# Kernel optimization log

Measured on AMD Instinct MI355X. Metric: run time of the kernel, lower is better.

Reference implementation:

```python
import jax, jax.numpy as jnp
import numpy as np

N_AA = 20
A = 15
D_FEAT = 128
CA_IDX = 1
NUM_FUNCS = 3
FREQ_BANDS = jnp.array([1.0, 2.0, 3.0, 1.0, 0.5, 1.0 / 3.0], dtype=jnp.float32)


def setup_inputs() -> dict:
    key = jax.random.key(0)
    ks = jax.random.split(key, 16)
    b, L = 16, 1024
    d_in = D_FEAT + N_AA * A * 3 + 3 * (NUM_FUNCS * 2 * 2 + 1) + D_FEAT  # 1195
    inp = {
        "seq": jax.random.randint(ks[0], (b, L), 0, N_AA),
        "xyz": jax.random.normal(ks[1], (b, L, A, 3), dtype=jnp.float32),
        "dihedrals": jax.random.normal(ks[2], (b, L, 3), dtype=jnp.float32),
        "chain_idx": jax.random.randint(ks[3], (b, L), 0, 10),
        "orientation": jax.random.normal(ks[4], (b, L, 3, 3), dtype=jnp.float32),
        "atom_mask": jnp.ones((b, L, A), dtype=bool),
        "aa_emb": jax.random.normal(ks[5], (N_AA, D_FEAT), dtype=jnp.float32),
        "chain_emb": jax.random.normal(ks[6], (10, D_FEAT), dtype=jnp.float32).at[0].set(0.0),  # padding_idx=0
        "W1": jax.random.normal(ks[7], (d_in, 2 * D_FEAT), dtype=jnp.float32) * 0.02,
        "b1": jnp.zeros((2 * D_FEAT,), dtype=jnp.float32),
        "W2": jax.random.normal(ks[8], (2 * D_FEAT, D_FEAT), dtype=jnp.float32) * 0.02,
        "b2": jnp.zeros((D_FEAT,), dtype=jnp.float32),
        "W3": jax.random.normal(ks[9], (D_FEAT, D_FEAT), dtype=jnp.float32) * 0.02,
        "b3": jnp.zeros((D_FEAT,), dtype=jnp.float32),
        "W4": jax.random.normal(ks[10], (D_FEAT, D_FEAT), dtype=jnp.float32) * 0.02,
        "b4": jnp.zeros((D_FEAT,), dtype=jnp.float32),
    }
    return inp


def angular_encoding(x):
    # x: (..., d_in) -> (..., d_in * 13)
    xe = x[..., None]  # (..., d_in, 1)
    enc = jnp.concatenate([xe, jnp.sin(FREQ_BANDS * xe), jnp.cos(FREQ_BANDS * xe)], axis=-1)
    return enc.reshape(*x.shape[:-1], -1)


def reference(seq, xyz, dihedrals, chain_idx, orientation, atom_mask,
              aa_emb, chain_emb, W1, b1, W2, b2, W3, b3, W4, b4):
    b, L = seq.shape
    aa_type_feat = aa_emb[seq]  # (b, L, d_feat)

    # local coordinates relative to CA, rotated into local frame via O^T
    xyz_rel = xyz - xyz[:, :, CA_IDX:CA_IDX + 1, :]  # (b, L, A, 3)
    xyz_local = jnp.einsum('blji,blaj->blai', orientation, xyz_rel)  # O^T @ xyz_rel

    # one-hot select: place xyz_local in the slot of the residue's aa type
    onehot = jax.nn.one_hot(seq, N_AA, dtype=xyz.dtype)  # (b, L, 20)
    coord_feat = (onehot[:, :, :, None, None] * xyz_local[:, :, None, :, :]).reshape(b, L, N_AA * A * 3)

    dihedral_feat = angular_encoding(dihedrals)  # (b, L, 39)

    chain_feat = chain_emb[chain_idx] * (chain_idx != 0)[..., None].astype(xyz.dtype)  # padding_idx=0

    x = jnp.concatenate([aa_type_feat, coord_feat, dihedral_feat, chain_feat], axis=-1)
    h = jax.nn.relu(x @ W1 + b1)
    h = jax.nn.relu(h @ W2 + b2)
    h = jax.nn.relu(h @ W3 + b3)
    return h @ W4 + b4
```

## Files before the change

kernel.cpp:

```cpp
#include <hip/hip_runtime.h>
#include <math.h>

#define N_AA    20
#define NATOM   15
#define TM      16
#define MAXBL   16384
#define MAXBLK  (MAXBL / TM + N_AA)
#define NWAVE   16

#define FSX  104
#define HSX  264
#define H2SX 136

typedef __attribute__((ext_vector_type(8))) short bf16x8;
typedef __attribute__((ext_vector_type(4))) float f32x4;

#define W1F_SLOTS  (N_AA * 16 * 3 * 64)
#define W2F_SLOTS  (8 * 8 * 64)
#define W34F_SLOTS (8 * 4 * 64)
#define TOT_SLOTS  (W1F_SLOTS + W2F_SLOTS + 2 * W34F_SLOTS)

__device__ __forceinline__ unsigned short f2bf(float x) {
    unsigned u = __float_as_uint(x);
    return (unsigned short)((u + 0x7FFFu + ((u >> 16) & 1u)) >> 16);
}
__device__ __forceinline__ float bf2f(unsigned short h) {
    return __uint_as_float(((unsigned)h) << 16);
}
__device__ __forceinline__ void put2(unsigned short* H, unsigned short* L, int idx, float v) {
    unsigned short hi = f2bf(v);
    H[idx] = hi;
    L[idx] = f2bf(v - bf2f(hi));
}

__global__ __launch_bounds__(1024) void prep_kernel(
    const int* __restrict__ seq, const float* __restrict__ aa_emb,
    const float* __restrict__ chain_emb, const float* __restrict__ W1,
    const float* __restrict__ W2, const float* __restrict__ W3, const float* __restrict__ W4,
    int BL,
    float* __restrict__ aaT, float* __restrict__ chT,
    int* __restrict__ bucket_start, int* __restrict__ blk_type,
    int* __restrict__ blk_chunk, int* __restrict__ rowidx,
    unsigned short* __restrict__ W1fH, unsigned short* __restrict__ W1fL,
    unsigned short* __restrict__ W2fH, unsigned short* __restrict__ W2fL,
    unsigned short* __restrict__ W3fH, unsigned short* __restrict__ W3fL,
    unsigned short* __restrict__ W4fH, unsigned short* __restrict__ W4fL)
{
    const int t = threadIdx.x;
    const int b = blockIdx.x;

    if (b < 8) {
        const int tab = b * 4 + (t >> 8);
        const int col = t & 255;
        if (tab < 30) {
            if (tab < N_AA) {
                const float* e = aa_emb + tab * 128;
                float acc = 0.f;
                #pragma unroll 8
                for (int k = 0; k < 128; ++k)
                    acc += e[k] * W1[(size_t)k * 256 + col];
                aaT[tab * 256 + col] = acc;
            } else {
                const int c = tab - N_AA;
                const float* e = chain_emb + c * 128;
                float acc = 0.f;
                #pragma unroll 8
                for (int k = 0; k < 128; ++k)
                    acc += e[k] * W1[(size_t)(1067 + k) * 256 + col];
                chT[c * 256 + col] = acc;
            }
        }
        return;
    }

    if (b >= 9) {
        const int slot = (b - 9) * 1024 + t;
        if (slot >= TOT_SLOTS) return;
        float v[8];
        unsigned short *dH, *dL;
        if (slot < W1F_SLOTS) {
            const int g = slot / 3072, r1 = slot % 3072;
            const int tile = r1 / 192, chunk = (r1 / 64) % 3, lane = r1 % 64;
            const int n  = tile * 16 + (lane & 15);
            const int kb = chunk * 32 + (lane >> 4) * 8;
            #pragma unroll
            for (int j = 0; j < 8; ++j) {
                const int k = kb + j;
                float x = 0.f;
                if (k < 45)       x = W1[(size_t)(128 + g * 45 + k) * 256 + n];
                else if (k < 84)  x = W1[(size_t)(1028 + k - 45) * 256 + n];
                v[j] = x;
            }
            dH = W1fH + (size_t)slot * 8; dL = W1fL + (size_t)slot * 8;
        } else if (slot < W1F_SLOTS + W2F_SLOTS) {
            const int s = slot - W1F_SLOTS;
            const int tile = s / 512, chunk = (s / 64) % 8, lane = s % 64;
            const int n  = tile * 16 + (lane & 15);
            const int kb = chunk * 32 + (lane >> 4) * 8;
            #pragma unroll
            for (int j = 0; j < 8; ++j) v[j] = W2[(size_t)(kb + j) * 128 + n];
            dH = W2fH + (size_t)s * 8; dL = W2fL + (size_t)s * 8;
        } else if (slot < W1F_SLOTS + W2F_SLOTS + W34F_SLOTS) {
            const int s = slot - W1F_SLOTS - W2F_SLOTS;
            const int tile = s / 256, chunk = (s / 64) % 4, lane = s % 64;
            const int n  = tile * 16 + (lane & 15);
            const int kb = chunk * 32 + (lane >> 4) * 8;
            #pragma unroll
            for (int j = 0; j < 8; ++j) v[j] = W3[(size_t)(kb + j) * 128 + n];
            dH = W3fH + (size_t)s * 8; dL = W3fL + (size_t)s * 8;
        } else {
            const int s = slot - W1F_SLOTS - W2F_SLOTS - W34F_SLOTS;
            const int tile = s / 256, chunk = (s / 64) % 4, lane = s % 64;
            const int n  = tile * 16 + (lane & 15);
            const int kb = chunk * 32 + (lane >> 4) * 8;
            #pragma unroll
            for (int j = 0; j < 8; ++j) v[j] = W4[(size_t)(kb + j) * 128 + n];
            dH = W4fH + (size_t)s * 8; dL = W4fL + (size_t)s * 8;
        }
        #pragma unroll
        for (int j = 0; j < 8; ++j) {
            const unsigned short hi = f2bf(v[j]);
            dH[j] = hi;
            dL[j] = f2bf(v[j] - bf2f(hi));
        }
        return;
    }

    __shared__ int sseq[MAXBL];
    __shared__ int hist[NWAVE][N_AA];
    __shared__ int wcur[NWAVE][N_AA];
    __shared__ int bs[N_AA + 1];
    __shared__ int blkoff[N_AA + 1];

    const int w = t >> 6;
    for (int i = t; i < BL; i += 1024) sseq[i] = seq[i];
    if (t < NWAVE * N_AA) hist[t / N_AA][t % N_AA] = 0;
    __syncthreads();
    for (int i = t; i < BL; i += 1024) atomicAdd(&hist[w][sseq[i]], 1);
    __syncthreads();
    if (t == 0) {
        int runr = 0, runb = 0;
        for (int g = 0; g < N_AA; ++g) {
            int s = 0;
            #pragma unroll
            for (int ww = 0; ww < NWAVE; ++ww) s += hist[ww][g];
            bs[g] = runr; runr += s;
            blkoff[g] = runb; runb += (s + TM - 1) / TM;
        }
        bs[N_AA] = runr; blkoff[N_AA] = runb;
    }
    __syncthreads();
    if (t <= N_AA) bucket_start[t] = bs[t];
    if (t < NWAVE * N_AA) {
        const int w2 = t / N_AA, g2 = t % N_AA;
        int o = bs[g2];
        for (int ww = 0; ww < w2; ++ww) o += hist[ww][g2];
        wcur[w2][g2] = o;
    }
    const int nblk = blkoff[N_AA];
    for (int i = t; i < MAXBLK; i += 1024) {
        if (i < nblk) {
            int g = 0;
            while (blkoff[g + 1] <= i) ++g;
            blk_type[i]  = g;
            blk_chunk[i] = i - blkoff[g];
        } else blk_type[i] = -1;
    }
    __syncthreads();
    for (int i = t; i < BL; i += 1024) {
        const int pos = atomicAdd(&wcur[w][sseq[i]], 1);
        rowidx[pos] = i;
    }
}

__global__ __launch_bounds__(256, 5) void fused_kernel(
    const int* __restrict__ chain_idx, const float* __restrict__ xyz,
    const float* __restrict__ dihedrals, const float* __restrict__ orientation,
    const float* __restrict__ b1, const float* __restrict__ b2,
    const float* __restrict__ b3, const float* __restrict__ b4,
    const float* __restrict__ aaT, const float* __restrict__ chT,
    const int* __restrict__ bucket_start, const int* __restrict__ blk_type,
    const int* __restrict__ blk_chunk, const int* __restrict__ rowidx,
    const unsigned short* __restrict__ W1fH, const unsigned short* __restrict__ W1fL,
    const unsigned short* __restrict__ W2fH, const unsigned short* __restrict__ W2fL,
    const unsigned short* __restrict__ W3fH, const unsigned short* __restrict__ W3fL,
    const unsigned short* __restrict__ W4fH, const unsigned short* __restrict__ W4fL,
    float* __restrict__ out)
{
    __shared__ __align__(16) unsigned short smemA[2 * TM * HSX];
    __shared__ __align__(16) unsigned short smemB[2 * TM * H2SX];
    __shared__ int s_row[TM], s_rowld[TM], s_chain[TM];

    unsigned short* hAH   = smemA;
    unsigned short* hAL   = smemA + TM * HSX;
    unsigned short* featH = smemB;
    unsigned short* featL = smemB + TM * FSX;
    unsigned short* hBH   = smemB;
    unsigned short* hBL   = smemB + TM * H2SX;

    const int t = threadIdx.x;
    const int g = blk_type[blockIdx.x];
    if (g < 0) return;
    const int chunk  = blk_chunk[blockIdx.x];
    const int bstart = bucket_start[g] + chunk * TM;
    const int nrows  = min(TM, bucket_start[g + 1] - bstart);

    if (t < TM) {
        const bool valid = (t < nrows);
        const int rl = rowidx[valid ? (bstart + t) : bstart];
        s_row[t]   = valid ? rl : -1;
        s_rowld[t] = rl;
        s_chain[t] = chain_idx[rl];
    }
    __syncthreads();

    if (t < TM * NATOM) {
        const int r = t / NATOM, a = t % NATOM;
        const int rl = s_rowld[r];
        const float* xr = xyz + (size_t)rl * (NATOM * 3);
        const float cax = xr[3], cay = xr[4], caz = xr[5];
        const float rx = xr[a*3+0] - cax;
        const float ry = xr[a*3+1] - cay;
        const float rz = xr[a*3+2] - caz;
        const float* O = orientation + (size_t)rl * 9;
        put2(featH, featL, r * FSX + a*3 + 0, O[0]*rx + O[3]*ry + O[6]*rz);
        put2(featH, featL, r * FSX + a*3 + 1, O[1]*rx + O[4]*ry + O[7]*rz);
        put2(featH, featL, r * FSX + a*3 + 2, O[2]*rx + O[5]*ry + O[8]*rz);
    }
    if (t < TM * 3) {
        const int r = t / 3, d = t % 3;
        const float x = dihedrals[(size_t)s_rowld[r] * 3 + d];
        const int base = r * FSX + 45 + d * 13;
        const float F3 = (float)(1.0 / 3.0);
        const float s1 = sinf(x), c1 = cosf(x);
        put2(featH, featL, base + 0, x);
        put2(featH, featL, base + 1, s1);           put2(featH, featL, base + 2, sinf(2.f*x));
        put2(featH, featL, base + 3, sinf(3.f*x));  put2(featH, featL, base + 4, s1);
        put2(featH, featL, base + 5, sinf(0.5f*x)); put2(featH, featL, base + 6, sinf(F3*x));
        put2(featH, featL, base + 7, c1);           put2(featH, featL, base + 8, cosf(2.f*x));
        put2(featH, featL, base + 9, cosf(3.f*x));  put2(featH, featL, base +10, c1);
        put2(featH, featL, base +11, cosf(0.5f*x)); put2(featH, featL, base +12, cosf(F3*x));
    }
    if (t < TM) {
        #pragma unroll
        for (int k = 84; k < 96; ++k) { featH[t * FSX + k] = 0; featL[t * FSX + k] = 0; }
    }
    __syncthreads();

    const int wave = t >> 6, lane = t & 63, quad = lane >> 4, nid = lane & 15;
    const f32x4 zero = {0.f, 0.f, 0.f, 0.f};

    {
        f32x4 acc[4] = {zero, zero, zero, zero};
        for (int c = 0; c < 3; ++c) {
            const bf16x8 aH = *(const bf16x8*)(featH + nid * FSX + c * 32 + quad * 8);
            const bf16x8 aL = *(const bf16x8*)(featL + nid * FSX + c * 32 + quad * 8);
            #pragma unroll
            for (int tt = 0; tt < 4; ++tt) {
                const size_t off = ((size_t)((g * 16 + (wave * 4 + tt)) * 3 + c) * 64 + lane) * 8;
                const bf16x8 bH = *(const bf16x8*)(W1fH + off);
                const bf16x8 bL = *(const bf16x8*)(W1fL + off);
                acc[tt] = __builtin_amdgcn_mfma_f32_16x16x32_bf16(aH, bH, acc[tt], 0, 0, 0);
                acc[tt] = __builtin_amdgcn_mfma_f32_16x16x32_bf16(aH, bL, acc[tt], 0, 0, 0);
                acc[tt] = __builtin_amdgcn_mfma_f32_16x16x32_bf16(aL, bH, acc[tt], 0, 0, 0);
            }
        }
        #pragma unroll
        for (int tt = 0; tt < 4; ++tt) {
            const int j = (wave * 4 + tt) * 16 + nid;
            const float cb = b1[j] + aaT[g * 256 + j];
            #pragma unroll
            for (int r = 0; r < 4; ++r) {
                const int row = quad * 4 + r;
                float v = acc[tt][r] + cb + chT[s_chain[row] * 256 + j];
                v = fmaxf(v, 0.f);
                put2(hAH, hAL, row * HSX + j, v);
            }
        }
    }
    __syncthreads();

    {
        f32x4 acc[2] = {zero, zero};
        for (int c = 0; c < 8; ++c) {
            const bf16x8 aH = *(const bf16x8*)(hAH + nid * HSX + c * 32 + quad * 8);
            const bf16x8 aL = *(const bf16x8*)(hAL + nid * HSX + c * 32 + quad * 8);
            #pragma unroll
            for (int tt = 0; tt < 2; ++tt) {
                const size_t off = ((size_t)((wave * 2 + tt) * 8 + c) * 64 + lane) * 8;
                const bf16x8 bH = *(const bf16x8*)(W2fH + off);
                const bf16x8 bL = *(const bf16x8*)(W2fL + off);
                acc[tt] = __builtin_amdgcn_mfma_f32_16x16x32_bf16(aH, bH, acc[tt], 0, 0, 0);
                acc[tt] = __builtin_amdgcn_mfma_f32_16x16x32_bf16(aH, bL, acc[tt], 0, 0, 0);
                acc[tt] = __builtin_amdgcn_mfma_f32_16x16x32_bf16(aL, bH, acc[tt], 0, 0, 0);
            }
        }
        __syncthreads();
        #pragma unroll
        for (int tt = 0; tt < 2; ++tt) {
            const int j = (wave * 2 + tt) * 16 + nid;
            const float bb = b2[j];
            #pragma unroll
            for (int r = 0; r < 4; ++r) {
                const int row = quad * 4 + r;
                float v = fmaxf(acc[tt][r] + bb, 0.f);
                put2(hBH, hBL, row * H2SX + j, v);
            }
        }
    }
    __syncthreads();

    {
        f32x4 acc[2] = {zero, zero};
        for (int c = 0; c < 4; ++c) {
            const bf16x8 aH = *(const bf16x8*)(hBH + nid * H2SX + c * 32 + quad * 8);
            const bf16x8 aL = *(const bf16x8*)(hBL + nid * H2SX + c * 32 + quad * 8);
            #pragma unroll
            for (int tt = 0; tt < 2; ++tt) {
                const size_t off = ((size_t)((wave * 2 + tt) * 4 + c) * 64 + lane) * 8;
                const bf16x8 bH = *(const bf16x8*)(W3fH + off);
                const bf16x8 bL = *(const bf16x8*)(W3fL + off);
                acc[tt] = __builtin_amdgcn_mfma_f32_16x16x32_bf16(aH, bH, acc[tt], 0, 0, 0);
                acc[tt] = __builtin_amdgcn_mfma_f32_16x16x32_bf16(aH, bL, acc[tt], 0, 0, 0);
                acc[tt] = __builtin_amdgcn_mfma_f32_16x16x32_bf16(aL, bH, acc[tt], 0, 0, 0);
            }
        }
        #pragma unroll
        for (int tt = 0; tt < 2; ++tt) {
            const int j = (wave * 2 + tt) * 16 + nid;
            const float bb = b3[j];
            #pragma unroll
            for (int r = 0; r < 4; ++r) {
                const int row = quad * 4 + r;
                float v = fmaxf(acc[tt][r] + bb, 0.f);
                put2(hAH, hAL, row * HSX + j, v);
            }
        }
    }
    __syncthreads();

    {
        f32x4 acc[2] = {zero, zero};
        for (int c = 0; c < 4; ++c) {
            const bf16x8 aH = *(const bf16x8*)(hAH + nid * HSX + c * 32 + quad * 8);
            const bf16x8 aL = *(const bf16x8*)(hAL + nid * HSX + c * 32 + quad * 8);
            #pragma unroll
            for (int tt = 0; tt < 2; ++tt) {
                const size_t off = ((size_t)((wave * 2 + tt) * 4 + c) * 64 + lane) * 8;
                const bf16x8 bH = *(const bf16x8*)(W4fH + off);
                const bf16x8 bL = *(const bf16x8*)(W4fL + off);
                acc[tt] = __builtin_amdgcn_mfma_f32_16x16x32_bf16(aH, bH, acc[tt], 0, 0, 0);
                acc[tt] = __builtin_amdgcn_mfma_f32_16x16x32_bf16(aH, bL, acc[tt], 0, 0, 0);
                acc[tt] = __builtin_amdgcn_mfma_f32_16x16x32_bf16(aL, bH, acc[tt], 0, 0, 0);
            }
        }
        #pragma unroll
        for (int tt = 0; tt < 2; ++tt) {
            const int j = (wave * 2 + tt) * 16 + nid;
            const float bb = b4[j];
            #pragma unroll
            for (int r = 0; r < 4; ++r) {
                const int row = quad * 4 + r;
                const int orow = s_row[row];
                if (orow >= 0) out[(size_t)orow * 128 + j] = acc[tt][r] + bb;
            }
        }
    }
}

extern "C" void kernel_launch(void* const* d_in, const int* in_sizes, int n_in,
                              void* d_out, int out_size, void* d_ws, size_t ws_size,
                              hipStream_t stream) {
    const int*   seq    = (const int*)d_in[0];
    const float* xyz    = (const float*)d_in[1];
    const float* dihed  = (const float*)d_in[2];
    const int*   chain  = (const int*)d_in[3];
    const float* orient = (const float*)d_in[4];
    const float* aa_emb = (const float*)d_in[6];
    const float* ch_emb = (const float*)d_in[7];
    const float* W1 = (const float*)d_in[8];
    const float* b1 = (const float*)d_in[9];
    const float* W2 = (const float*)d_in[10];
    const float* b2 = (const float*)d_in[11];
    const float* W3 = (const float*)d_in[12];
    const float* b3 = (const float*)d_in[13];
    const float* W4 = (const float*)d_in[14];
    const float* b4 = (const float*)d_in[15];
    float* out = (float*)d_out;

    const int BL = in_sizes[0];

    char* p = (char*)d_ws;
    float* aaT = (float*)p;            p += 20 * 256 * 4;
    float* chT = (float*)p;            p += 10 * 256 * 4;
    int* bucket_start = (int*)p;       p += 32 * 4;
    int* blk_type     = (int*)p;       p += MAXBLK * 4;
    int* blk_chunk    = (int*)p;       p += MAXBLK * 4;
    int* rowidx       = (int*)p;       p += MAXBL * 4;
    p += ((16 - ((uintptr_t)p & 15)) & 15);
    unsigned short* W1fH = (unsigned short*)p; p += (size_t)W1F_SLOTS * 8 * 2;
    unsigned short* W1fL = (unsigned short*)p; p += (size_t)W1F_SLOTS * 8 * 2;
    unsigned short* W2fH = (unsigned short*)p; p += (size_t)W2F_SLOTS * 8 * 2;
    unsigned short* W2fL = (unsigned short*)p; p += (size_t)W2F_SLOTS * 8 * 2;
    unsigned short* W3fH = (unsigned short*)p; p += (size_t)W34F_SLOTS * 8 * 2;
    unsigned short* W3fL = (unsigned short*)p; p += (size_t)W34F_SLOTS * 8 * 2;
    unsigned short* W4fH = (unsigned short*)p; p += (size_t)W34F_SLOTS * 8 * 2;
    unsigned short* W4fL = (unsigned short*)p;

    const int nprep  = 9 + (TOT_SLOTS + 1023) / 1024;
    const int nfused = BL / TM + N_AA;

    prep_kernel<<<nprep, 1024, 0, stream>>>(seq, aa_emb, ch_emb, W1, W2, W3, W4, BL,
                                            aaT, chT, bucket_start, blk_type, blk_chunk, rowidx,
                                            W1fH, W1fL, W2fH, W2fL, W3fH, W3fL, W4fH, W4fL);
    fused_kernel<<<nfused, 256, 0, stream>>>(chain, xyz, dihed, orient,
                                             b1, b2, b3, b4, aaT, chT,
                                             bucket_start, blk_type, blk_chunk, rowidx,
                                             W1fH, W1fL, W2fH, W2fL, W3fH, W3fL, W4fH, W4fL,
                                             out);
}
```

Before: 124.4 us.

## Double row tile to 32 and reuse weight fragments across two row tiles

Raises the per-block row tile from 16 to 32 and the block size from 256 to 512 threads (8 waves). Each wave now loads each weight fragment once and applies it to two 16-row A tiles, with the column tiles redistributed across waves in every layer. The aim is to halve global/L2 weight traffic per output row and cut the number of blocks. The cost is more padded rows per amino-acid bucket, doubled shared memory per block, and higher register pressure from the doubled accumulators.

After: 124.2 us. No clear change (-0.2%).

```diff
diff --git a/kernel.cpp b/kernel.cpp
--- a/kernel.cpp
+++ b/kernel.cpp
@@ -3,7 +3,7 @@
 
 #define N_AA    20
 #define NATOM   15
-#define TM      16
+#define TM      32
 #define MAXBL   16384
 #define MAXBLK  (MAXBL / TM + N_AA)
 #define NWAVE   16
@@ -173,7 +173,7 @@
     }
 }
 
-__global__ __launch_bounds__(256, 5) void fused_kernel(
+__global__ __launch_bounds__(512, 4) void fused_kernel(
     const int* __restrict__ chain_idx, const float* __restrict__ xyz,
     const float* __restrict__ dihedrals, const float* __restrict__ orientation,
     const float* __restrict__ b1, const float* __restrict__ b2,
@@ -251,30 +251,38 @@
     const f32x4 zero = {0.f, 0.f, 0.f, 0.f};
 
     {
-        f32x4 acc[4] = {zero, zero, zero, zero};
+        f32x4 acc[2][2] = {{zero, zero}, {zero, zero}};
         for (int c = 0; c < 3; ++c) {
-            const bf16x8 aH = *(const bf16x8*)(featH + nid * FSX + c * 32 + quad * 8);
-            const bf16x8 aL = *(const bf16x8*)(featL + nid * FSX + c * 32 + quad * 8);
-            #pragma unroll
-            for (int tt = 0; tt < 4; ++tt) {
-                const size_t off = ((size_t)((g * 16 + (wave * 4 + tt)) * 3 + c) * 64 + lane) * 8;
+            const bf16x8 aH0 = *(const bf16x8*)(featH + nid * FSX + c * 32 + quad * 8);
+            const bf16x8 aL0 = *(const bf16x8*)(featL + nid * FSX + c * 32 + quad * 8);
+            const bf16x8 aH1 = *(const bf16x8*)(featH + (16 + nid) * FSX + c * 32 + quad * 8);
+            const bf16x8 aL1 = *(const bf16x8*)(featL + (16 + nid) * FSX + c * 32 + quad * 8);
+            #pragma unroll
+            for (int tt = 0; tt < 2; ++tt) {
+                const size_t off = ((size_t)((g * 16 + (wave * 2 + tt)) * 3 + c) * 64 + lane) * 8;
                 const bf16x8 bH = *(const bf16x8*)(W1fH + off);
                 const bf16x8 bL = *(const bf16x8*)(W1fL + off);
-                acc[tt] = __builtin_amdgcn_mfma_f32_16x16x32_bf16(aH, bH, acc[tt], 0, 0, 0);
-                acc[tt] = __builtin_amdgcn_mfma_f32_16x16x32_bf16(aH, bL, acc[tt], 0, 0, 0);
-                acc[tt] = __builtin_amdgcn_mfma_f32_16x16x32_bf16(aL, bH, acc[tt], 0, 0, 0);
-            }
-        }
-        #pragma unroll
-        for (int tt = 0; tt < 4; ++tt) {
-            const int j = (wave * 4 + tt) * 16 + nid;
+                acc[0][tt] = __builtin_amdgcn_mfma_f32_16x16x32_bf16(aH0, bH, acc[0][tt], 0, 0, 0);
+                acc[0][tt] = __builtin_amdgcn_mfma_f32_16x16x32_bf16(aH0, bL, acc[0][tt], 0, 0, 0);
+                acc[0][tt] = __builtin_amdgcn_mfma_f32_16x16x32_bf16(aL0, bH, acc[0][tt], 0, 0, 0);
+                acc[1][tt] = __builtin_amdgcn_mfma_f32_16x16x32_bf16(aH1, bH, acc[1][tt], 0, 0, 0);
+                acc[1][tt] = __builtin_amdgcn_mfma_f32_16x16x32_bf16(aH1, bL, acc[1][tt], 0, 0, 0);
+                acc[1][tt] = __builtin_amdgcn_mfma_f32_16x16x32_bf16(aL1, bH, acc[1][tt], 0, 0, 0);
+            }
+        }
+        #pragma unroll
+        for (int tt = 0; tt < 2; ++tt) {
+            const int j = (wave * 2 + tt) * 16 + nid;
             const float cb = b1[j] + aaT[g * 256 + j];
             #pragma unroll
-            for (int r = 0; r < 4; ++r) {
-                const int row = quad * 4 + r;
-                float v = acc[tt][r] + cb + chT[s_chain[row] * 256 + j];
-                v = fmaxf(v, 0.f);
-                put2(hAH, hAL, row * HSX + j, v);
+            for (int rt = 0; rt < 2; ++rt) {
+                #pragma unroll
+                for (int r = 0; r < 4; ++r) {
+                    const int row = rt * 16 + quad * 4 + r;
+                    float v = acc[rt][tt][r] + cb + chT[s_chain[row] * 256 + j];
+                    v = fmaxf(v, 0.f);
+                    put2(hAH, hAL, row * HSX + j, v);
+                }
             }
         }
     }
@@ -283,27 +291,29 @@
     {
         f32x4 acc[2] = {zero, zero};
         for (int c = 0; c < 8; ++c) {
-            const bf16x8 aH = *(const bf16x8*)(hAH + nid * HSX + c * 32 + quad * 8);
-            const bf16x8 aL = *(const bf16x8*)(hAL + nid * HSX + c * 32 + quad * 8);
-            #pragma unroll
-            for (int tt = 0; tt < 2; ++tt) {
-                const size_t off = ((size_t)((wave * 2 + tt) * 8 + c) * 64 + lane) * 8;
-                const bf16x8 bH = *(const bf16x8*)(W2fH + off);
-                const bf16x8 bL = *(const bf16x8*)(W2fL + off);
-                acc[tt] = __builtin_amdgcn_mfma_f32_16x16x32_bf16(aH, bH, acc[tt], 0, 0, 0);
-                acc[tt] = __builtin_amdgcn_mfma_f32_16x16x32_bf16(aH, bL, acc[tt], 0, 0, 0);
-                acc[tt] = __builtin_amdgcn_mfma_f32_16x16x32_bf16(aL, bH, acc[tt], 0, 0, 0);
-            }
+            const bf16x8 aH0 = *(const bf16x8*)(hAH + nid * HSX + c * 32 + quad * 8);
+            const bf16x8 aL0 = *(const bf16x8*)(hAL + nid * HSX + c * 32 + quad * 8);
+            const bf16x8 aH1 = *(const bf16x8*)(hAH + (16 + nid) * HSX + c * 32 + quad * 8);
+            const bf16x8 aL1 = *(const bf16x8*)(hAL + (16 + nid) * HSX + c * 32 + quad * 8);
+            const size_t off = ((size_t)(wave * 8 + c) * 64 + lane) * 8;
+            const bf16x8 bH = *(const bf16x8*)(W2fH + off);
+            const bf16x8 bL = *(const bf16x8*)(W2fL + off);
+            acc[0] = __builtin_amdgcn_mfma_f32_16x16x32_bf16(aH0, bH, acc[0], 0, 0, 0);
+            acc[0] = __builtin_amdgcn_mfma_f32_16x16x32_bf16(aH0, bL, acc[0], 0, 0, 0);
+            acc[0] = __builtin_amdgcn_mfma_f32_16x16x32_bf16(aL0, bH, acc[0], 0, 0, 0);
+            acc[1] = __builtin_amdgcn_mfma_f32_16x16x32_bf16(aH1, bH, acc[1], 0, 0, 0);
+            acc[1] = __builtin_amdgcn_mfma_f32_16x16x32_bf16(aH1, bL, acc[1], 0, 0, 0);
+            acc[1] = __builtin_amdgcn_mfma_f32_16x16x32_bf16(aL1, bH, acc[1], 0, 0, 0);
         }
         __syncthreads();
-        #pragma unroll
-        for (int tt = 0; tt < 2; ++tt) {
-            const int j = (wave * 2 + tt) * 16 + nid;
-            const float bb = b2[j];
+        const int j = wave * 16 + nid;
+        const float bb = b2[j];
+        #pragma unroll
+        for (int rt = 0; rt < 2; ++rt) {
             #pragma unroll
             for (int r = 0; r < 4; ++r) {
-                const int row = quad * 4 + r;
-                float v = fmaxf(acc[tt][r] + bb, 0.f);
+                const int row = rt * 16 + quad * 4 + r;
+                float v = fmaxf(acc[rt][r] + bb, 0.f);
                 put2(hBH, hBL, row * H2SX + j, v);
             }
         }
@@ -313,26 +323,28 @@
     {
         f32x4 acc[2] = {zero, zero};
         for (int c = 0; c < 4; ++c) {
-            const bf16x8 aH = *(const bf16x8*)(hBH + nid * H2SX + c * 32 + quad * 8);
-            const bf16x8 aL = *(const bf16x8*)(hBL + nid * H2SX + c * 32 + quad * 8);
-            #pragma unroll
-            for (int tt = 0; tt < 2; ++tt) {
-                const size_t off = ((size_t)((wave * 2 + tt) * 4 + c) * 64 + lane) * 8;
-                const bf16x8 bH = *(const bf16x8*)(W3fH + off);
-                const bf16x8 bL = *(const bf16x8*)(W3fL + off);
-                acc[tt] = __builtin_amdgcn_mfma_f32_16x16x32_bf16(aH, bH, acc[tt], 0, 0, 0);
-                acc[tt] = __builtin_amdgcn_mfma_f32_16x16x32_bf16(aH, bL, acc[tt], 0, 0, 0);
-                acc[tt] = __builtin_amdgcn_mfma_f32_16x16x32_bf16(aL, bH, acc[tt], 0, 0, 0);
-            }
-        }
-        #pragma unroll
-        for (int tt = 0; tt < 2; ++tt) {
-            const int j = (wave * 2 + tt) * 16 + nid;
-            const float bb = b3[j];
+            const bf16x8 aH0 = *(const bf16x8*)(hBH + nid * H2SX + c * 32 + quad * 8);
+            const bf16x8 aL0 = *(const bf16x8*)(hBL + nid * H2SX + c * 32 + quad * 8);
+            const bf16x8 aH1 = *(const bf16x8*)(hBH + (16 + nid) * H2SX + c * 32 + quad * 8);
+            const bf16x8 aL1 = *(const bf16x8*)(hBL + (16 + nid) * H2SX + c * 32 + quad * 8);
+            const size_t off = ((size_t)(wave * 4 + c) * 64 + lane) * 8;
+            const bf16x8 bH = *(const bf16x8*)(W3fH + off);
+            const bf16x8 bL = *(const bf16x8*)(W3fL + off);
+            acc[0] = __builtin_amdgcn_mfma_f32_16x16x32_bf16(aH0, bH, acc[0], 0, 0, 0);
+            acc[0] = __builtin_amdgcn_mfma_f32_16x16x32_bf16(aH0, bL, acc[0], 0, 0, 0);
+            acc[0] = __builtin_amdgcn_mfma_f32_16x16x32_bf16(aL0, bH, acc[0], 0, 0, 0);
+            acc[1] = __builtin_amdgcn_mfma_f32_16x16x32_bf16(aH1, bH, acc[1], 0, 0, 0);
+            acc[1] = __builtin_amdgcn_mfma_f32_16x16x32_bf16(aH1, bL, acc[1], 0, 0, 0);
+            acc[1] = __builtin_amdgcn_mfma_f32_16x16x32_bf16(aL1, bH, acc[1], 0, 0, 0);
+        }
+        const int j = wave * 16 + nid;
+        const float bb = b3[j];
+        #pragma unroll
+        for (int rt = 0; rt < 2; ++rt) {
             #pragma unroll
             for (int r = 0; r < 4; ++r) {
-                const int row = quad * 4 + r;
-                float v = fmaxf(acc[tt][r] + bb, 0.f);
+                const int row = rt * 16 + quad * 4 + r;
+                float v = fmaxf(acc[rt][r] + bb, 0.f);
                 put2(hAH, hAL, row * HSX + j, v);
             }
         }
@@ -342,27 +354,29 @@
     {
         f32x4 acc[2] = {zero, zero};
         for (int c = 0; c < 4; ++c) {
-            const bf16x8 aH = *(const bf16x8*)(hAH + nid * HSX + c * 32 + quad * 8);
-            const bf16x8 aL = *(const bf16x8*)(hAL + nid * HSX + c * 32 + quad * 8);
-            #pragma unroll
-            for (int tt = 0; tt < 2; ++tt) {
-                const size_t off = ((size_t)((wave * 2 + tt) * 4 + c) * 64 + lane) * 8;
-                const bf16x8 bH = *(const bf16x8*)(W4fH + off);
-                const bf16x8 bL = *(const bf16x8*)(W4fL + off);
-                acc[tt] = __builtin_amdgcn_mfma_f32_16x16x32_bf16(aH, bH, acc[tt], 0, 0, 0);
-                acc[tt] = __builtin_amdgcn_mfma_f32_16x16x32_bf16(aH, bL, acc[tt], 0, 0, 0);
-                acc[tt] = __builtin_amdgcn_mfma_f32_16x16x32_bf16(aL, bH, acc[tt], 0, 0, 0);
-            }
-        }
-        #pragma unroll
-        for (int tt = 0; tt < 2; ++tt) {
-            const int j = (wave * 2 + tt) * 16 + nid;
-            const float bb = b4[j];
+            const bf16x8 aH0 = *(const bf16x8*)(hAH + nid * HSX + c * 32 + quad * 8);
+            const bf16x8 aL0 = *(const bf16x8*)(hAL + nid * HSX + c * 32 + quad * 8);
+            const bf16x8 aH1 = *(const bf16x8*)(hAH + (16 + nid) * HSX + c * 32 + quad * 8);
+            const bf16x8 aL1 = *(const bf16x8*)(hAL + (16 + nid) * HSX + c * 32 + quad * 8);
+            const size_t off = ((size_t)(wave * 4 + c) * 64 + lane) * 8;
+            const bf16x8 bH = *(const bf16x8*)(W4fH + off);
+            const bf16x8 bL = *(const bf16x8*)(W4fL + off);
+            acc[0] = __builtin_amdgcn_mfma_f32_16x16x32_bf16(aH0, bH, acc[0], 0, 0, 0);
+            acc[0] = __builtin_amdgcn_mfma_f32_16x16x32_bf16(aH0, bL, acc[0], 0, 0, 0);
+            acc[0] = __builtin_amdgcn_mfma_f32_16x16x32_bf16(aL0, bH, acc[0], 0, 0, 0);
+            acc[1] = __builtin_amdgcn_mfma_f32_16x16x32_bf16(aH1, bH, acc[1], 0, 0, 0);
+            acc[1] = __builtin_amdgcn_mfma_f32_16x16x32_bf16(aH1, bL, acc[1], 0, 0, 0);
+            acc[1] = __builtin_amdgcn_mfma_f32_16x16x32_bf16(aL1, bH, acc[1], 0, 0, 0);
+        }
+        const int j = wave * 16 + nid;
+        const float bb = b4[j];
+        #pragma unroll
+        for (int rt = 0; rt < 2; ++rt) {
             #pragma unroll
             for (int r = 0; r < 4; ++r) {
-                const int row = quad * 4 + r;
+                const int row = rt * 16 + quad * 4 + r;
                 const int orow = s_row[row];
-                if (orow >= 0) out[(size_t)orow * 128 + j] = acc[tt][r] + bb;
+                if (orow >= 0) out[(size_t)orow * 128 + j] = acc[rt][r] + bb;
             }
         }
     }
@@ -413,7 +427,7 @@
     prep_kernel<<<nprep, 1024, 0, stream>>>(seq, aa_emb, ch_emb, W1, W2, W3, W4, BL,
                                             aaT, chT, bucket_start, blk_type, blk_chunk, rowidx,
                                             W1fH, W1fL, W2fH, W2fL, W3fH, W3fL, W4fH, W4fL);
-    fused_kernel<<<nfused, 256, 0, stream>>>(chain, xyz, dihed, orient,
+    fused_kernel<<<nfused, 512, 0, stream>>>(chain, xyz, dihed, orient,
                                              b1, b2, b3, b4, aaT, chT,
                                              bucket_start, blk_type, blk_chunk, rowidx,
                                              W1fH, W1fL, W2fH, W2fL, W3fH, W3fL, W4fH, W4fL,
```
